# Performance work log

Hardware: AMD Instinct MI355X
Metric: run time of the kernel (lower is better)

The kernel has to match this reference:

```python
import jax, jax.numpy as jnp
import numpy as np

B, C, N, K, O = 8, 64, 4096, 20, 64
EPS = 1e-5


def setup_inputs() -> dict:
    key = jax.random.key(0)
    k1, k2, k3 = jax.random.split(key, 3)
    x = jax.random.normal(k1, (B, C, N), dtype=jnp.float32)
    # Conv2d(2C, O, kernel_size=1) -> weight [O, 2C], bias [O]
    fan_in = 2 * C
    bound = 1.0 / np.sqrt(fan_in)
    W = jax.random.uniform(k2, (O, 2 * C), minval=-bound, maxval=bound, dtype=jnp.float32)
    b = jax.random.uniform(k3, (O,), minval=-bound, maxval=bound, dtype=jnp.float32)
    gamma = jnp.ones((O,), dtype=jnp.float32)
    beta = jnp.zeros((O,), dtype=jnp.float32)
    return {"x": x, "W": W, "b": b, "gamma": gamma, "beta": beta}


def reference(x, W, b, gamma, beta):
    k = K
    Bs, Cs, Ns = x.shape
    x_t = jnp.transpose(x, (0, 2, 1))  # [B, N, C]
    # pairwise squared distances (monotonic with cdist, same topk indices)
    sq = jnp.sum(x_t * x_t, axis=-1)  # [B, N]
    d2 = sq[:, :, None] + sq[:, None, :] - 2.0 * jnp.einsum("bnc,bmc->bnm", x_t, x_t)
    valid_k = min(k, Ns - 1)
    _, idx = jax.lax.top_k(-d2, valid_k + 1)  # smallest distances
    idx = idx[:, :, 1:]  # drop self -> [B, N, k]
    # gather neighbor features per batch
    nbr = jax.vmap(lambda xt, i: xt[i])(x_t, idx)  # [B, N, k, C]
    central = x_t[:, :, None, :]  # [B, N, 1, C]
    edge = jnp.concatenate(
        [jnp.broadcast_to(central, (Bs, Ns, k, Cs)), nbr - central], axis=-1
    )  # [B, N, k, 2C]
    # 1x1 conv == channel matmul
    y = jnp.einsum("bnkc,oc->bonk", edge, W) + b[None, :, None, None]  # [B, O, N, k]
    # BatchNorm2d in training mode: batch statistics over (B, N, k)
    mean = jnp.mean(y, axis=(0, 2, 3), keepdims=True)
    var = jnp.var(y, axis=(0, 2, 3), keepdims=True)
    yn = (y - mean) * jax.lax.rsqrt(var + EPS)
    yn = gamma[None, :, None, None] * yn + beta[None, :, None, None]
    out = jax.nn.relu(yn)
    return jnp.max(out, axis=-1)  # [B, O, N]
```

## Files before the change

### kernel.cpp

```cpp
#include <hip/hip_runtime.h>
#include <hip/hip_bf16.h>

#define BB 8
#define CC 64
#define NN 4096
#define KK 20
#define OO 64
#define FMAXV 3.402823466e38f

typedef __attribute__((ext_vector_type(8))) short short8;
typedef __attribute__((ext_vector_type(4))) float f32x4;

__global__ __launch_bounds__(256) void kprep(const float* __restrict__ x,
                                             const float* __restrict__ W,
                                             const float* __restrict__ bias,
                                             float* __restrict__ xt,
                                             unsigned short* __restrict__ xb,
                                             float* __restrict__ sq,
                                             float* __restrict__ u,
                                             float* __restrict__ v) {
  __shared__ float tile[64][65];
  const int b = blockIdx.y, n0 = blockIdx.x * 64;
  const int lane = threadIdx.x & 63, grp = threadIdx.x >> 6;
  #pragma unroll
  for (int j = 0; j < 16; ++j) {
    int c = grp + j * 4;
    tile[c][lane] = x[((size_t)b * CC + c) * NN + n0 + lane];
  }
  float w2r[64], wdr[64];
  const float4* W4 = (const float4*)W;
  #pragma unroll
  for (int c4 = 0; c4 < 16; ++c4) {
    float4 q1 = W4[lane * 32 + c4];
    float4 q2 = W4[lane * 32 + 16 + c4];
    w2r[c4*4]=q2.x; w2r[c4*4+1]=q2.y; w2r[c4*4+2]=q2.z; w2r[c4*4+3]=q2.w;
    wdr[c4*4]=q1.x-q2.x; wdr[c4*4+1]=q1.y-q2.y; wdr[c4*4+2]=q1.z-q2.z; wdr[c4*4+3]=q1.w-q2.w;
  }
  const float bo = bias[lane];
  __syncthreads();
  #pragma unroll
  for (int j = 0; j < 16; ++j) {
    int n = grp + j * 4;
    float vv = tile[lane][n];
    size_t off = ((size_t)b * NN + n0 + n) * CC + lane;
    xt[off] = vv;
    unsigned int uu = __builtin_bit_cast(unsigned int, vv);
    xb[off] = (unsigned short)((uu + 0x7FFFu + ((uu >> 16) & 1u)) >> 16);
  }
  if (threadIdx.x < 64) {
    float s = 0.f;
    #pragma unroll
    for (int c = 0; c < 64; ++c) { float vv = tile[c][lane]; s += vv * vv; }
    sq[(size_t)b * NN + n0 + lane] = s;
  }
  for (int j = 0; j < 16; ++j) {
    int nl = grp * 16 + j;
    float du = 0.f, dv = 0.f;
    #pragma unroll
    for (int c = 0; c < 64; ++c) {
      float xv = tile[c][nl];
      du += w2r[c] * xv;
      dv += wdr[c] * xv;
    }
    size_t off = ((size_t)b * NN + n0 + nl) * OO + lane;
    u[off] = du;
    v[off] = dv + bo;
  }
}

__device__ __forceinline__ int lanes_below(unsigned long long m) {
  unsigned lo = (unsigned)m, hi = (unsigned)(m >> 32);
  int c = __builtin_amdgcn_mbcnt_lo(lo, 0);
  return (int)__builtin_amdgcn_mbcnt_hi(hi, (unsigned)c);
}

__device__ __forceinline__ unsigned packkey(float d, int m) {
  unsigned u = __builtin_bit_cast(unsigned, d);
  u ^= ((int)u < 0) ? 0xFFFFFFFFu : 0x80000000u;
  return (u & 0xFFFFF000u) | (unsigned)m;
}

__device__ __forceinline__ float unpackkey(unsigned t) {
  unsigned u = t | 0xFFFu;
  u = (u & 0x80000000u) ? (u ^ 0x80000000u) : ~u;
  return __builtin_bit_cast(float, u);
}

__device__ __forceinline__ unsigned bitonic64(unsigned v, int lane) {
  #pragma unroll
  for (int k = 2; k <= 64; k <<= 1) {
    #pragma unroll
    for (int j = k >> 1; j >= 1; j >>= 1) {
      unsigned o = (unsigned)__shfl_xor((int)v, j);
      bool up    = ((lane & k) == 0);
      bool lower = ((lane & j) == 0);
      unsigned mn = (v < o) ? v : o;
      unsigned mx = (v < o) ? o : v;
      v = (up == lower) ? mn : mx;
    }
  }
  return v;
}

__global__ __launch_bounds__(256, 4) void kknn6(const unsigned short* __restrict__ xb,
                                                const float* __restrict__ sq,
                                                unsigned* __restrict__ kcand) {
  __shared__ unsigned slist[4][16][32];
  __shared__ unsigned sbuf[4][16][64];
  const int lane = threadIdx.x & 63, w = threadIdx.x >> 6;
  const int wid = blockIdx.x * 4 + w;
  const int b = wid >> 9;
  const int half = (wid >> 8) & 1;
  const int n0g = (wid & 255) * 16;
  const int ch0 = half * (NN / 2);
  const int l15 = lane & 15, q = lane >> 4;
  const unsigned long long qmask = 0xFFFFull << (q * 16);

  const unsigned short* xbB = xb + (size_t)b * NN * CC;
  const float* sqB = sq + (size_t)b * NN;

  #pragma unroll
  for (int i = 0; i < 8; ++i) {
    int idx = i * 64 + lane;
    slist[w][idx >> 5][idx & 31] = 0xFFFFFFFFu;
  }

  short8 afr[2];
  #pragma unroll
  for (int ks = 0; ks < 2; ++ks)
    afr[ks] = __builtin_bit_cast(short8, *(const int4*)(xbB + (size_t)(n0g + l15) * CC + ks * 32 + q * 8));

  float tauf4[4];
  int cnt4[4], done4[4];
  #pragma unroll
  for (int j = 0; j < 4; ++j) { tauf4[j] = FMAXV; cnt4[j] = 0; done4[j] = 0; }

  for (int t = 0; t < 32; ++t) {
    const int cb = ch0 + t * 64;
    short8 bfr[4][2];
    float sv[4];
    #pragma unroll
    for (int ct = 0; ct < 4; ++ct) {
      #pragma unroll
      for (int ks = 0; ks < 2; ++ks)
        bfr[ct][ks] = __builtin_bit_cast(short8,
            *(const int4*)(xbB + (size_t)(cb + ct * 16 + l15) * CC + ks * 32 + q * 8));
      sv[ct] = sqB[cb + ct * 16 + l15];
    }
    f32x4 acc[4];
    #pragma unroll
    for (int ct = 0; ct < 4; ++ct) {
      acc[ct] = (f32x4){0.f, 0.f, 0.f, 0.f};
      acc[ct] = __builtin_amdgcn_mfma_f32_16x16x32_bf16(afr[0], bfr[ct][0], acc[ct], 0, 0, 0);
      acc[ct] = __builtin_amdgcn_mfma_f32_16x16x32_bf16(afr[1], bfr[ct][1], acc[ct], 0, 0, 0);
    }

    #pragma unroll
    for (int ct = 0; ct < 4; ++ct) {
      const int colg = cb + ct * 16 + l15;
      float dj[4];
      bool pj[4];
      #pragma unroll
      for (int j = 0; j < 4; ++j) {
        float d = sv[ct] - 2.f * acc[ct][j];
        if (colg == n0g + q * 4 + j) d = FMAXV;
        dj[j] = d;
        pj[j] = d <= tauf4[j];
      }
      if (!__ballot(pj[0] | pj[1] | pj[2] | pj[3])) continue;
      #pragma unroll
      for (int j = 0; j < 4; ++j) {
        unsigned long long bal = __ballot(pj[j]);
        if (!bal) continue;
        const int rowl = q * 4 + j;
        int posq = lanes_below(bal & qmask);
        if (pj[j]) sbuf[w][rowl][(cnt4[j] + posq) & 63] = packkey(dj[j], colg);
        cnt4[j] += __popcll(bal & qmask);
        unsigned long long mb = __ballot(cnt4[j] - done4[j] >= 32);
        while (mb) {
          int src = __ffsll(mb) - 1;
          int qm = src >> 4;
          int rowm = qm * 4 + j;
          int dsrc = __shfl(done4[j], src);
          unsigned v = (lane < 32) ? slist[w][rowm][lane]
                                   : sbuf[w][rowm][(dsrc + lane - 32) & 63];
          v = bitonic64(v, lane);
          if (lane < 32) slist[w][rowm][lane] = v;
          unsigned tn = (unsigned)__shfl((int)v, 31);
          if (q == qm) { tauf4[j] = unpackkey(tn); done4[j] += 32; }
          mb &= ~(0xFFFFull << (qm * 16));
        }
      }
    }
  }

  #pragma unroll
  for (int j = 0; j < 4; ++j) {
    unsigned long long mb = __ballot(cnt4[j] > done4[j]);
    while (mb) {
      int src = __ffsll(mb) - 1;
      int qm = src >> 4;
      int rowm = qm * 4 + j;
      int dsrc = __shfl(done4[j], src);
      int csrc = __shfl(cnt4[j], src);
      int rem = csrc - dsrc;
      unsigned v = (lane < 32) ? slist[w][rowm][lane]
                 : ((lane - 32) < rem ? sbuf[w][rowm][(dsrc + lane - 32) & 63] : 0xFFFFFFFFu);
      v = bitonic64(v, lane);
      if (lane < 32) slist[w][rowm][lane] = v;
      if (q == qm) done4[j] = cnt4[j];
      mb &= ~(0xFFFFull << (qm * 16));
    }
  }

  unsigned* kc = kcand + (((size_t)b * 2 + half) * NN + n0g) * 32;
  #pragma unroll
  for (int i = 0; i < 8; ++i) {
    int idx = i * 64 + lane;
    kc[idx] = slist[w][idx >> 5][idx & 31];
  }
}

__global__ __launch_bounds__(256) void kpost(const unsigned* __restrict__ kcand,
                                             const float* __restrict__ xt,
                                             const float* __restrict__ sq,
                                             const float* __restrict__ u,
                                             const float* __restrict__ v,
                                             float* __restrict__ umax,
                                             float* __restrict__ umin,
                                             float* __restrict__ gS) {
  const int lane = threadIdx.x & 63, w = threadIdx.x >> 6;
  const int gw = blockIdx.x * 4 + w;
  const int hl = lane & 31;
  float s1 = 0.f, s2 = 0.f;

  for (int it = 0; it < 2; ++it) {
    const int rbase = gw * 4 + it * 2;
    const int b = rbase >> 12;
    const int n = rbase & (NN - 1);

    const unsigned* kc0 = kcand + (((size_t)b * 2 + 0) * NN) * 32;
    const unsigned* kc1 = kcand + (((size_t)b * 2 + 1) * NN) * 32;
    unsigned vA = (lane < 32) ? kc0[(size_t)n * 32 + lane] : kc1[(size_t)n * 32 + (lane - 32)];
    vA = bitonic64(vA, lane);
    unsigned vB = (lane < 32) ? kc0[(size_t)(n + 1) * 32 + lane] : kc1[(size_t)(n + 1) * 32 + (lane - 32)];
    vB = bitonic64(vB, lane);
    unsigned kx = (unsigned)__shfl_xor((int)vB, 32);
    unsigned key = (lane < 32) ? vA : kx;
    int m = (int)(key & 0xFFFu);
    const int rowg = n + ((lane >= 32) ? 1 : 0);

    const float* xtB = xt + (size_t)b * NN * CC;
    const float* sqB = sq + (size_t)b * NN;
    const float4* pr = (const float4*)(xtB + (size_t)rowg * CC);
    const float4* pm = (const float4*)(xtB + (size_t)m * CC);
    float t0 = 0.f, t1 = 0.f, t2 = 0.f, t3 = 0.f;
    #pragma unroll
    for (int i = 0; i < 16; ++i) {
      float4 a = pr[i], c = pm[i];
      t0 += a.x * c.x; t1 += a.y * c.y; t2 += a.z * c.z; t3 += a.w * c.w;
    }
    float ev = sqB[m] - 2.f * ((t0 + t1) + (t2 + t3));

    #pragma unroll
    for (int k = 2; k <= 32; k <<= 1) {
      #pragma unroll
      for (int jj = k >> 1; jj >= 1; jj >>= 1) {
        float e2 = __shfl_xor(ev, jj);
        int   m2 = __shfl_xor(m, jj);
        bool up    = ((hl & k) == 0);
        bool lower = ((hl & jj) == 0);
        bool less  = (e2 < ev) || (e2 == ev && m2 < m);
        bool take  = (up == lower) ? less : !less;
        if (take) { ev = e2; m = m2; }
      }
    }

    const float* uB = u + (size_t)b * NN * OO;
    #pragma unroll
    for (int rr = 0; rr < 2; ++rr) {
      const int rown = n + rr;
      float vv = v[((size_t)b * NN + rown) * OO + lane];
      float mx = -FMAXV, mn = FMAXV;
      #pragma unroll
      for (int k = 0; k < KK; ++k) {
        int id = __shfl(m, rr * 32 + k);
        float uu = uB[(size_t)id * OO + lane];
        float y = vv + uu;
        s1 += y; s2 += y * y;
        mx = fmaxf(mx, uu); mn = fminf(mn, uu);
      }
      umax[((size_t)b * NN + rown) * OO + lane] = mx;
      umin[((size_t)b * NN + rown) * OO + lane] = mn;
    }
  }

  __shared__ float r1[4][64], r2[4][64];
  r1[w][lane] = s1; r2[w][lane] = s2;
  __syncthreads();
  if (w == 0) {
    float a = r1[0][lane] + r1[1][lane] + r1[2][lane] + r1[3][lane];
    float c = r2[0][lane] + r2[1][lane] + r2[2][lane] + r2[3][lane];
    float* g = gS + (blockIdx.x & 7) * 128;
    atomicAdd(&g[lane], a);
    atomicAdd(&g[64 + lane], c);
  }
}

__global__ __launch_bounds__(256) void kout(const float* __restrict__ v,
                                            const float* __restrict__ umax,
                                            const float* __restrict__ umin,
                                            const float* __restrict__ gS,
                                            const float* __restrict__ gamma,
                                            const float* __restrict__ beta,
                                            float* __restrict__ out) {
  __shared__ float sA[64], sB[64];
  __shared__ float zt[64][65];
  const int b = blockIdx.y, n0 = blockIdx.x * 64;
  const int lane = threadIdx.x & 63, w = threadIdx.x >> 6;
  if (threadIdx.x < 64) {
    float s1 = 0.f, s2 = 0.f;
    #pragma unroll
    for (int rsub = 0; rsub < 8; ++rsub) {
      s1 += gS[rsub * 128 + lane];
      s2 += gS[rsub * 128 + 64 + lane];
    }
    const float cnt = (float)BB * NN * KK;
    float m  = s1 / cnt;
    float var = s2 / cnt - m * m;
    float A = gamma[lane] * rsqrtf(var + 1e-5f);
    sA[lane] = A;
    sB[lane] = beta[lane] - A * m;
  }
  __syncthreads();
  for (int j = 0; j < 16; ++j) {
    int nl = w * 16 + j;
    size_t off = ((size_t)b * NN + n0 + nl) * OO + lane;
    float A = sA[lane];
    float c0 = A * v[off] + sB[lane];
    float z = c0 + A * ((A > 0.f) ? umax[off] : umin[off]);
    zt[nl][lane] = fmaxf(z, 0.f);
  }
  __syncthreads();
  for (int j = 0; j < 16; ++j) {
    int o = w * 16 + j;
    out[((size_t)b * OO + o) * NN + n0 + lane] = zt[lane][o];
  }
}

extern "C" void kernel_launch(void* const* d_in, const int* in_sizes, int n_in,
                              void* d_out, int out_size, void* d_ws, size_t ws_size,
                              hipStream_t stream) {
  const float* x     = (const float*)d_in[0];
  const float* W     = (const float*)d_in[1];
  const float* bias  = (const float*)d_in[2];
  const float* gamma = (const float*)d_in[3];
  const float* beta  = (const float*)d_in[4];
  float* out = (float*)d_out;

  float* xt  = (float*)d_ws;
  float* sq  = xt  + (size_t)BB*NN*CC;
  float* u   = sq  + (size_t)BB*NN;
  float* v   = u   + (size_t)BB*NN*OO;
  float* umx = v   + (size_t)BB*NN*OO;
  float* umn = umx + (size_t)BB*NN*OO;
  float* gS  = umn + (size_t)BB*NN*OO;
  unsigned short* xb = (unsigned short*)(gS + 1024);
  unsigned* kcand = (unsigned*)(xb + (size_t)BB*NN*CC);

  hipMemsetAsync(gS, 0, 1024 * sizeof(float), stream);
  kprep<<<dim3(NN/64, BB), 256, 0, stream>>>(x, W, bias, xt, xb, sq, u, v);
  kknn6<<<dim3(1024),      256, 0, stream>>>(xb, sq, kcand);
  kpost<<<dim3(2048),      256, 0, stream>>>(kcand, xt, sq, u, v, umx, umn, gS);
  kout <<<dim3(NN/64, BB), 256, 0, stream>>>(v, umx, umn, gS, gamma, beta, out);
}
```

Before: 418.8 us.

## Batch candidate insertion per row and drop self-mask in KNN kernel

The KNN candidate loop now iterates per row and issues four ballots at once, appending up to 64 candidates per row before checking whether to merge. The staging buffer doubles to 128 entries to hold the larger batches. The explicit self-distance mask is removed, so self is kept as the nearest candidate and the post kernel skips index 0 instead. This cuts per-column-tile ballot and branch overhead, at the cost of more shared memory per block, which may lower occupancy, and a reliance on self always sorting first.

```diff
diff --git a/kernel.cpp b/kernel.cpp
--- a/kernel.cpp
+++ b/kernel.cpp
@@ -102,11 +102,11 @@
   return v;
 }
 
-__global__ __launch_bounds__(256, 4) void kknn6(const unsigned short* __restrict__ xb,
+__global__ __launch_bounds__(256, 4) void kknn7(const unsigned short* __restrict__ xb,
                                                 const float* __restrict__ sq,
                                                 unsigned* __restrict__ kcand) {
   __shared__ unsigned slist[4][16][32];
-  __shared__ unsigned sbuf[4][16][64];
+  __shared__ unsigned sbuf[4][16][128];
   const int lane = threadIdx.x & 63, w = threadIdx.x >> 6;
   const int wid = blockIdx.x * 4 + w;
   const int b = wid >> 9;
@@ -156,40 +156,60 @@
     }
 
     #pragma unroll
-    for (int ct = 0; ct < 4; ++ct) {
-      const int colg = cb + ct * 16 + l15;
-      float dj[4];
-      bool pj[4];
+    for (int j = 0; j < 4; ++j) {
+      float dv[4];
+      bool  pj[4];
       #pragma unroll
-      for (int j = 0; j < 4; ++j) {
-        float d = sv[ct] - 2.f * acc[ct][j];
-        if (colg == n0g + q * 4 + j) d = FMAXV;
-        dj[j] = d;
-        pj[j] = d <= tauf4[j];
-      }
-      if (!__ballot(pj[0] | pj[1] | pj[2] | pj[3])) continue;
-      #pragma unroll
-      for (int j = 0; j < 4; ++j) {
-        unsigned long long bal = __ballot(pj[j]);
-        if (!bal) continue;
-        const int rowl = q * 4 + j;
-        int posq = lanes_below(bal & qmask);
-        if (pj[j]) sbuf[w][rowl][(cnt4[j] + posq) & 63] = packkey(dj[j], colg);
-        cnt4[j] += __popcll(bal & qmask);
+      for (int ct = 0; ct < 4; ++ct) {
+        dv[ct] = sv[ct] - 2.f * acc[ct][j];
+        pj[ct] = dv[ct] <= tauf4[j];
+      }
+      unsigned long long b0 = __ballot(pj[0]);
+      unsigned long long b1 = __ballot(pj[1]);
+      unsigned long long b2 = __ballot(pj[2]);
+      unsigned long long b3 = __ballot(pj[3]);
+      if (!(b0 | b1 | b2 | b3)) continue;
+
+      const int rowl = q * 4 + j;
+      int base = cnt4[j];
+      {
+        unsigned long long bq = b0 & qmask;
+        if (pj[0]) sbuf[w][rowl][(base + lanes_below(bq)) & 127] = packkey(dv[0], cb + 0 * 16 + l15);
+        base += __popcll(bq);
+      }
+      {
+        unsigned long long bq = b1 & qmask;
+        if (pj[1]) sbuf[w][rowl][(base + lanes_below(bq)) & 127] = packkey(dv[1], cb + 1 * 16 + l15);
+        base += __popcll(bq);
+      }
+      {
+        unsigned long long bq = b2 & qmask;
+        if (pj[2]) sbuf[w][rowl][(base + lanes_below(bq)) & 127] = packkey(dv[2], cb + 2 * 16 + l15);
+        base += __popcll(bq);
+      }
+      {
+        unsigned long long bq = b3 & qmask;
+        if (pj[3]) sbuf[w][rowl][(base + lanes_below(bq)) & 127] = packkey(dv[3], cb + 3 * 16 + l15);
+        base += __popcll(bq);
+      }
+      cnt4[j] = base;
+
+      for (;;) {
         unsigned long long mb = __ballot(cnt4[j] - done4[j] >= 32);
-        while (mb) {
+        if (!mb) break;
+        do {
           int src = __ffsll(mb) - 1;
           int qm = src >> 4;
           int rowm = qm * 4 + j;
           int dsrc = __shfl(done4[j], src);
           unsigned v = (lane < 32) ? slist[w][rowm][lane]
-                                   : sbuf[w][rowm][(dsrc + lane - 32) & 63];
+                                   : sbuf[w][rowm][(dsrc + lane - 32) & 127];
           v = bitonic64(v, lane);
           if (lane < 32) slist[w][rowm][lane] = v;
           unsigned tn = (unsigned)__shfl((int)v, 31);
           if (q == qm) { tauf4[j] = unpackkey(tn); done4[j] += 32; }
           mb &= ~(0xFFFFull << (qm * 16));
-        }
+        } while (mb);
       }
     }
   }
@@ -205,7 +225,7 @@
       int csrc = __shfl(cnt4[j], src);
       int rem = csrc - dsrc;
       unsigned v = (lane < 32) ? slist[w][rowm][lane]
-                 : ((lane - 32) < rem ? sbuf[w][rowm][(dsrc + lane - 32) & 63] : 0xFFFFFFFFu);
+                 : ((lane - 32) < rem ? sbuf[w][rowm][(dsrc + lane - 32) & 127] : 0xFFFFFFFFu);
       v = bitonic64(v, lane);
       if (lane < 32) slist[w][rowm][lane] = v;
       if (q == qm) done4[j] = cnt4[j];
@@ -284,7 +304,7 @@
       float mx = -FMAXV, mn = FMAXV;
       #pragma unroll
       for (int k = 0; k < KK; ++k) {
-        int id = __shfl(m, rr * 32 + k);
+        int id = __shfl(m, rr * 32 + 1 + k);
         float uu = uB[(size_t)id * OO + lane];
         float y = vv + uu;
         s1 += y; s2 += y * y;
@@ -370,7 +390,7 @@
 
   hipMemsetAsync(gS, 0, 1024 * sizeof(float), stream);
   kprep<<<dim3(NN/64, BB), 256, 0, stream>>>(x, W, bias, xt, xb, sq, u, v);
-  kknn6<<<dim3(1024),      256, 0, stream>>>(xb, sq, kcand);
+  kknn7<<<dim3(1024),      256, 0, stream>>>(xb, sq, kcand);
   kpost<<<dim3(2048),      256, 0, stream>>>(kcand, xt, sq, u, v, umx, umn, gS);
   kout <<<dim3(NN/64, BB), 256, 0, stream>>>(v, umx, umn, gS, gamma, beta, out);
 }
```

New measurement: 404.5 us. -3.4%, faster.

## Split KNN candidate scan into four column quarters and merge with bitonic merges

Applied to the files above, without the earlier changes.

The KNN kernel now splits the candidate columns into four quarters instead of two, doubling the grid and raising the occupancy hint, with a smaller 48-entry ring buffer per row. Self-exclusion is dropped from the scan; the post kernel merges four sorted 32-candidate lists with bitonic merge steps (reversed second halves) instead of full sorts, then skips the first entry as the self match. This aims for more parallelism and cheaper merging. The cost is twice the candidate storage and reads, and correctness now depends on the point itself always ranking first.

```diff
diff --git a/kernel.cpp b/kernel.cpp
--- a/kernel.cpp
+++ b/kernel.cpp
@@ -102,17 +102,28 @@
   return v;
 }
 
-__global__ __launch_bounds__(256, 4) void kknn6(const unsigned short* __restrict__ xb,
+__device__ __forceinline__ unsigned merge6(unsigned v, int lane) {
+  #pragma unroll
+  for (int j = 32; j >= 1; j >>= 1) {
+    unsigned o = (unsigned)__shfl_xor((int)v, j);
+    unsigned mn = (v < o) ? v : o;
+    unsigned mx = (v < o) ? o : v;
+    v = ((lane & j) == 0) ? mn : mx;
+  }
+  return v;
+}
+
+__global__ __launch_bounds__(256, 8) void kknn8(const unsigned short* __restrict__ xb,
                                                 const float* __restrict__ sq,
                                                 unsigned* __restrict__ kcand) {
   __shared__ unsigned slist[4][16][32];
-  __shared__ unsigned sbuf[4][16][64];
+  __shared__ unsigned sbuf[4][16][48];
   const int lane = threadIdx.x & 63, w = threadIdx.x >> 6;
   const int wid = blockIdx.x * 4 + w;
-  const int b = wid >> 9;
-  const int half = (wid >> 8) & 1;
+  const int b = wid >> 10;
+  const int quarter = (wid >> 8) & 3;
   const int n0g = (wid & 255) * 16;
-  const int ch0 = half * (NN / 2);
+  const int ch0 = quarter * (NN / 4);
   const int l15 = lane & 15, q = lane >> 4;
   const unsigned long long qmask = 0xFFFFull << (q * 16);
 
@@ -131,11 +142,11 @@
     afr[ks] = __builtin_bit_cast(short8, *(const int4*)(xbB + (size_t)(n0g + l15) * CC + ks * 32 + q * 8));
 
   float tauf4[4];
-  int cnt4[4], done4[4];
-  #pragma unroll
-  for (int j = 0; j < 4; ++j) { tauf4[j] = FMAXV; cnt4[j] = 0; done4[j] = 0; }
-
-  for (int t = 0; t < 32; ++t) {
+  int o4[4], w4[4], r4[4];
+  #pragma unroll
+  for (int j = 0; j < 4; ++j) { tauf4[j] = FMAXV; o4[j] = 0; w4[j] = 0; r4[j] = 0; }
+
+  for (int t = 0; t < 16; ++t) {
     const int cb = ch0 + t * 64;
     short8 bfr[4][2];
     float sv[4];
@@ -156,38 +167,51 @@
     }
 
     #pragma unroll
-    for (int ct = 0; ct < 4; ++ct) {
-      const int colg = cb + ct * 16 + l15;
+    for (int j = 0; j < 4; ++j) {
       float dj[4];
-      bool pj[4];
+      bool  pj[4];
       #pragma unroll
-      for (int j = 0; j < 4; ++j) {
-        float d = sv[ct] - 2.f * acc[ct][j];
-        if (colg == n0g + q * 4 + j) d = FMAXV;
-        dj[j] = d;
-        pj[j] = d <= tauf4[j];
+      for (int ct = 0; ct < 4; ++ct) {
+        dj[ct] = sv[ct] - 2.f * acc[ct][j];
+        pj[ct] = dj[ct] <= tauf4[j];
       }
-      if (!__ballot(pj[0] | pj[1] | pj[2] | pj[3])) continue;
+      unsigned long long bl0 = __ballot(pj[0]);
+      unsigned long long bl1 = __ballot(pj[1]);
+      unsigned long long bl2 = __ballot(pj[2]);
+      unsigned long long bl3 = __ballot(pj[3]);
+      if (!(bl0 | bl1 | bl2 | bl3)) continue;
+
+      const int rowl = q * 4 + j;
       #pragma unroll
-      for (int j = 0; j < 4; ++j) {
-        unsigned long long bal = __ballot(pj[j]);
-        if (!bal) continue;
-        const int rowl = q * 4 + j;
-        int posq = lanes_below(bal & qmask);
-        if (pj[j]) sbuf[w][rowl][(cnt4[j] + posq) & 63] = packkey(dj[j], colg);
-        cnt4[j] += __popcll(bal & qmask);
-        unsigned long long mb = __ballot(cnt4[j] - done4[j] >= 32);
+      for (int ct = 0; ct < 4; ++ct) {
+        unsigned long long blc = (ct == 0) ? bl0 : (ct == 1) ? bl1 : (ct == 2) ? bl2 : bl3;
+        unsigned long long bq = blc & qmask;
+        int pos = lanes_below(bq);
+        int qc  = __popcll(bq);
+        if (pj[ct]) {
+          int idx = w4[j] + pos; if (idx >= 48) idx -= 48;
+          sbuf[w][rowl][idx] = packkey(dj[ct], cb + ct * 16 + l15);
+        }
+        w4[j] += qc; if (w4[j] >= 48) w4[j] -= 48;
+        o4[j] += qc;
+
+        unsigned long long mb = __ballot(o4[j] >= 32);
         while (mb) {
           int src = __ffsll(mb) - 1;
           int qm = src >> 4;
           int rowm = qm * 4 + j;
-          int dsrc = __shfl(done4[j], src);
+          int rsrc = __shfl(r4[j], src);
+          int ridx = rsrc + (lane - 32); if (ridx >= 48) ridx -= 48;
           unsigned v = (lane < 32) ? slist[w][rowm][lane]
-                                   : sbuf[w][rowm][(dsrc + lane - 32) & 63];
+                                   : sbuf[w][rowm][ridx];
           v = bitonic64(v, lane);
           if (lane < 32) slist[w][rowm][lane] = v;
           unsigned tn = (unsigned)__shfl((int)v, 31);
-          if (q == qm) { tauf4[j] = unpackkey(tn); done4[j] += 32; }
+          if (q == qm) {
+            tauf4[j] = unpackkey(tn);
+            r4[j] += 32; if (r4[j] >= 48) r4[j] -= 48;
+            o4[j] -= 32;
+          }
           mb &= ~(0xFFFFull << (qm * 16));
         }
       }
@@ -196,29 +220,44 @@
 
   #pragma unroll
   for (int j = 0; j < 4; ++j) {
-    unsigned long long mb = __ballot(cnt4[j] > done4[j]);
+    unsigned long long mb = __ballot(o4[j] > 0);
     while (mb) {
       int src = __ffsll(mb) - 1;
       int qm = src >> 4;
       int rowm = qm * 4 + j;
-      int dsrc = __shfl(done4[j], src);
-      int csrc = __shfl(cnt4[j], src);
-      int rem = csrc - dsrc;
+      int rsrc = __shfl(r4[j], src);
+      int rem  = __shfl(o4[j], src);
+      int ridx = rsrc + (lane - 32); if (ridx >= 48) ridx -= 48;
       unsigned v = (lane < 32) ? slist[w][rowm][lane]
-                 : ((lane - 32) < rem ? sbuf[w][rowm][(dsrc + lane - 32) & 63] : 0xFFFFFFFFu);
+                 : ((lane - 32) < rem ? sbuf[w][rowm][ridx] : 0xFFFFFFFFu);
       v = bitonic64(v, lane);
       if (lane < 32) slist[w][rowm][lane] = v;
-      if (q == qm) done4[j] = cnt4[j];
+      if (q == qm) o4[j] = 0;
       mb &= ~(0xFFFFull << (qm * 16));
     }
   }
 
-  unsigned* kc = kcand + (((size_t)b * 2 + half) * NN + n0g) * 32;
+  unsigned* kc = kcand + (((size_t)b * 4 + quarter) * NN + n0g) * 32;
   #pragma unroll
   for (int i = 0; i < 8; ++i) {
     int idx = i * 64 + lane;
     kc[idx] = slist[w][idx >> 5][idx & 31];
   }
+}
+
+__device__ __forceinline__ unsigned preselect(const unsigned* __restrict__ kcB,
+                                              int row, int lane) {
+  const int li = (lane < 32) ? lane : (63 - lane);
+  unsigned v01 = (lane < 32) ? kcB[((size_t)0 * NN + row) * 32 + li]
+                             : kcB[((size_t)1 * NN + row) * 32 + li];
+  v01 = merge6(v01, lane);
+  unsigned v23 = (lane < 32) ? kcB[((size_t)2 * NN + row) * 32 + li]
+                             : kcB[((size_t)3 * NN + row) * 32 + li];
+  v23 = merge6(v23, lane);
+  unsigned sw = (unsigned)__shfl_xor((int)v23, 63);
+  unsigned vm = (lane < 32) ? v01 : sw;
+  vm = merge6(vm, lane);
+  return vm;
 }
 
 __global__ __launch_bounds__(256) void kpost(const unsigned* __restrict__ kcand,
@@ -239,14 +278,11 @@
     const int b = rbase >> 12;
     const int n = rbase & (NN - 1);
 
-    const unsigned* kc0 = kcand + (((size_t)b * 2 + 0) * NN) * 32;
-    const unsigned* kc1 = kcand + (((size_t)b * 2 + 1) * NN) * 32;
-    unsigned vA = (lane < 32) ? kc0[(size_t)n * 32 + lane] : kc1[(size_t)n * 32 + (lane - 32)];
-    vA = bitonic64(vA, lane);
-    unsigned vB = (lane < 32) ? kc0[(size_t)(n + 1) * 32 + lane] : kc1[(size_t)(n + 1) * 32 + (lane - 32)];
-    vB = bitonic64(vB, lane);
-    unsigned kx = (unsigned)__shfl_xor((int)vB, 32);
-    unsigned key = (lane < 32) ? vA : kx;
+    const unsigned* kcB = kcand + (size_t)b * 4 * NN * 32;
+    unsigned keyN  = preselect(kcB, n,     lane);
+    unsigned keyN1 = preselect(kcB, n + 1, lane);
+    unsigned kx = (unsigned)__shfl_xor((int)keyN1, 32);
+    unsigned key = (lane < 32) ? keyN : kx;
     int m = (int)(key & 0xFFFu);
     const int rowg = n + ((lane >= 32) ? 1 : 0);
 
@@ -284,7 +320,7 @@
       float mx = -FMAXV, mn = FMAXV;
       #pragma unroll
       for (int k = 0; k < KK; ++k) {
-        int id = __shfl(m, rr * 32 + k);
+        int id = __shfl(m, rr * 32 + 1 + k);
         float uu = uB[(size_t)id * OO + lane];
         float y = vv + uu;
         s1 += y; s2 += y * y;
@@ -370,7 +406,7 @@
 
   hipMemsetAsync(gS, 0, 1024 * sizeof(float), stream);
   kprep<<<dim3(NN/64, BB), 256, 0, stream>>>(x, W, bias, xt, xb, sq, u, v);
-  kknn6<<<dim3(1024),      256, 0, stream>>>(xb, sq, kcand);
+  kknn8<<<dim3(2048),      256, 0, stream>>>(xb, sq, kcand);
   kpost<<<dim3(2048),      256, 0, stream>>>(kcand, xt, sq, u, v, umx, umn, gS);
   kout <<<dim3(NN/64, BB), 256, 0, stream>>>(v, umx, umn, gS, gamma, beta, out);
 }
```

Measured after the change: 527.6 us. 1.26x slower.
